# Kernel optimization log

Hardware: AMD Instinct MI355X
Metric: run time of the kernel (lower is better)

The kernel has to match this reference:

```python
import jax, jax.numpy as jnp
import numpy as np

N_NODES = 100000
N_EDGES = 1600000
DIMS = [128, 128, 128, 64]


def setup_inputs() -> dict:
    key = jax.random.key(0)
    ks = jax.random.split(key, 12)
    inp = {
        "features": jax.random.normal(ks[0], (N_NODES, DIMS[0]), dtype=jnp.float32),
        "src": jax.random.randint(ks[1], (N_EDGES,), 0, N_NODES, dtype=jnp.int64),
        "dst": jax.random.randint(ks[2], (N_EDGES,), 0, N_NODES, dtype=jnp.int64),
        "edge_weight": jax.random.uniform(ks[3], (N_EDGES,), dtype=jnp.float32),
    }
    # GraphConv weights (xavier-like scale) and biases per layer
    for i in range(3):
        fin, fout = DIMS[i], DIMS[i + 1]
        scale = (2.0 / (fin + fout)) ** 0.5
        inp[f"W{i}"] = jax.random.normal(ks[4 + i], (fin, fout), dtype=jnp.float32) * scale
        inp[f"b{i}"] = jnp.zeros((fout,), dtype=jnp.float32)
    return inp


def _graph_conv(h, W, b, src, dst, ew, out_norm, in_norm):
    # DGL GraphConv, norm='both', with per-edge weight (u_mul_e message).
    fin, fout = W.shape
    h = h * out_norm[:, None]
    if fin > fout:  # mult W first to reduce message width
        h = h @ W
    msg = h[src] * ew[:, None]                       # [E, d] irregular gather
    agg = jax.ops.segment_sum(msg, dst, num_segments=N_NODES)
    agg = agg * in_norm[:, None]
    if fin <= fout:
        agg = agg @ W
    return agg + b


def reference(features, src, dst, edge_weight, W0, b0, W1, b1, W2, b2):
    ones = jnp.ones((N_EDGES,), dtype=features.dtype)
    out_deg = jax.ops.segment_sum(ones, src, num_segments=N_NODES)
    in_deg = jax.ops.segment_sum(ones, dst, num_segments=N_NODES)
    out_norm = jnp.clip(out_deg, 1.0, None) ** -0.5
    in_norm = jnp.clip(in_deg, 1.0, None) ** -0.5
    h = features
    Ws = [(W0, b0), (W1, b1), (W2, b2)]
    for i, (W, b) in enumerate(Ws):
        h = _graph_conv(h, W, b, src, dst, edge_weight, out_norm, in_norm)
        if i < len(Ws) - 1:
            h = jax.nn.relu(h)
    return h
```

## Files before the change

### kernel.cpp

```cpp
#include <hip/hip_runtime.h>
#include <cstddef>
#include <cstdint>

typedef float f4 __attribute__((ext_vector_type(4)));
typedef unsigned long long u64;
typedef unsigned short u16;
typedef unsigned char u8;
typedef unsigned short u16x8 __attribute__((ext_vector_type(8)));
typedef short short8 __attribute__((ext_vector_type(8)));

__device__ __forceinline__ u64 ldnt8(const void* p) {
    return __builtin_nontemporal_load((const u64*)(p));
}
__device__ __forceinline__ u16 bfrn(float f) {
    unsigned u = __float_as_uint(f);
    return (u16)((u + 0x7FFFu + ((u >> 16) & 1u)) >> 16);
}
__device__ __forceinline__ float bl(unsigned w) { return __uint_as_float(w << 16); }
__device__ __forceinline__ float bh(unsigned w) { return __uint_as_float(w & 0xFFFF0000u); }


#define EPB 4096

__global__ void __launch_bounds__(256)
k_prep0(const int* __restrict__ src, const int* __restrict__ dst,
        int* __restrict__ bh_s, int* __restrict__ bh_d,
        const float* __restrict__ feat, u16* __restrict__ featb, int n8,
        const float* __restrict__ W0, const float* __restrict__ W1,
        const float* __restrict__ W2, u16* __restrict__ Wt0,
        u16* __restrict__ Wt1, u16* __restrict__ Wt2,
        int NB, int B1, int E) {
    const int bid = blockIdx.x, t = threadIdx.x;
    if (bid < B1) {
        __shared__ int hs[512], hd[512];
        for (int i = t; i < 512; i += 256) { hs[i] = 0; hd[i] = 0; }
        __syncthreads();
        const int e0 = bid * EPB;
        #pragma unroll
        for (int j = 0; j < 4; ++j) {
            const int e = e0 + j * 1024 + t * 4;
            if (e + 4 <= E) {
                const int4 d = *(const int4*)&dst[e];
                const int4 s = *(const int4*)&src[e];
                atomicAdd(&hd[d.x >> 8], 1);
                atomicAdd(&hd[d.y >> 8], 1);
                atomicAdd(&hd[d.z >> 8], 1);
                atomicAdd(&hd[d.w >> 8], 1);
                atomicAdd(&hs[s.x >> 8], 1);
                atomicAdd(&hs[s.y >> 8], 1);
                atomicAdd(&hs[s.z >> 8], 1);
                atomicAdd(&hs[s.w >> 8], 1);
            } else {
                for (int k = e; k < E && k < e + 4; ++k) {
                    atomicAdd(&hd[dst[k] >> 8], 1);
                    atomicAdd(&hs[src[k] >> 8], 1);
                }
            }
        }
        __syncthreads();
        for (int i = t; i < NB; i += 256) {
            bh_d[bid * NB + i] = hd[i];
            bh_s[bid * NB + i] = hs[i];
        }
    } else if (bid < B1 + (n8 + 255) / 256) {
        const int i = (bid - B1) * 256 + t;
        if (i < n8) {
            const f4 v0 = *(const f4*)(feat + (size_t)i * 8);
            const f4 v1 = *(const f4*)(feat + (size_t)i * 8 + 4);
            u16x8 r = {bfrn(v0.x), bfrn(v0.y), bfrn(v0.z), bfrn(v0.w),
                       bfrn(v1.x), bfrn(v1.y), bfrn(v1.z), bfrn(v1.w)};
            *(u16x8*)(featb + (size_t)i * 8) = r;
        }
    } else {
        const int i = (bid - B1 - (n8 + 255) / 256) * 256 + t;
        if (i < 16384) {
            const int k = i >> 7, c = i & 127;
            Wt0[c * 128 + k] = bfrn(W0[i]);
        } else if (i < 32768) {
            const int j = i - 16384, k = j >> 7, c = j & 127;
            Wt1[c * 128 + k] = bfrn(W1[j]);
        } else if (i < 40960) {
            const int j = i - 32768, k = j >> 6, c = j & 63;
            Wt2[c * 128 + k] = bfrn(W2[j]);
        }
    }
}

__global__ void __launch_bounds__(512)
k_p2(int* __restrict__ bh_d, int* __restrict__ bh_s,
     int* __restrict__ cb_d, int* __restrict__ cb_s, int NB, int B1) {
    __shared__ int tile[512][17];
    __shared__ int tot[16];
    const int t = threadIdx.x, lane = t & 63, wave = t >> 6;
    int* bh = blockIdx.y ? bh_s : bh_d;
    int* cb = blockIdx.y ? cb_s : cb_d;
    const int B0 = blockIdx.x * 16;
    #pragma unroll
    for (int j = 0; j < 16; ++j) {
        const int idx = j * 512 + t;
        const int row = idx >> 4, col = idx & 15;
        int v = 0;
        if (row < B1 && B0 + col < NB) v = bh[row * NB + B0 + col];
        tile[row][col] = v;
    }
    __syncthreads();
    #pragma unroll
    for (int cc = 0; cc < 2; ++cc) {
        const int col = wave * 2 + cc;
        int carry = 0;
        #pragma unroll
        for (int ch = 0; ch < 8; ++ch) {
            const int v = tile[ch * 64 + lane][col];
            int s = v;
            #pragma unroll
            for (int d = 1; d < 64; d <<= 1) {
                const int u = __shfl_up(s, d);
                if (lane >= d) s += u;
            }
            tile[ch * 64 + lane][col] = s - v + carry;
            carry += __shfl(s, 63);
        }
        if (lane == 0) tot[col] = carry;
    }
    __syncthreads();
    #pragma unroll
    for (int j = 0; j < 16; ++j) {
        const int idx = j * 512 + t;
        const int row = idx >> 4, col = idx & 15;
        if (row < B1 && B0 + col < NB) bh[row * NB + B0 + col] = tile[row][col];
    }
    if (t < 16 && B0 + t < NB) cb[B0 + t] = tot[t];
}

__global__ void __launch_bounds__(512)
k_p2b(const int* __restrict__ cb_d, const int* __restrict__ cb_s,
      int* __restrict__ bktb_d, int* __restrict__ bktb_s,
      int* __restrict__ row, int NB, int N, int E) {
    __shared__ int s[512];
    const int t = threadIdx.x;
    int v = (t < NB) ? cb_d[t] : 0;
    s[t] = v;
    __syncthreads();
    for (int off = 1; off < 512; off <<= 1) {
        const int x = (t >= off) ? s[t - off] : 0;
        __syncthreads();
        s[t] += x;
        __syncthreads();
    }
    if (t < NB) bktb_d[t] = s[t] - v;
    __syncthreads();
    v = (t < NB) ? cb_s[t] : 0;
    s[t] = v;
    __syncthreads();
    for (int off = 1; off < 512; off <<= 1) {
        const int x = (t >= off) ? s[t - off] : 0;
        __syncthreads();
        s[t] += x;
        __syncthreads();
    }
    if (t < NB) bktb_s[t] = s[t] - v;
    if (t == 0) row[N] = E;
}

__global__ void __launch_bounds__(256)
k_p3(const int* __restrict__ src, const int* __restrict__ dst,
     const float* __restrict__ ew,
     const int* __restrict__ bh_s, const int* __restrict__ bh_d,
     const int* __restrict__ bktb_s, const int* __restrict__ bktb_d,
     int2* __restrict__ tsw, u8* __restrict__ tsrc, int NB, int E) {
    __shared__ int hs[512], hd[512], base_s[512], base_d[512];
    const int t = threadIdx.x, b = blockIdx.x;
    for (int i = t; i < 512; i += 256) {
        hs[i] = 0; hd[i] = 0;
        if (i < NB) {
            base_d[i] = bktb_d[i] + bh_d[b * NB + i];
            base_s[i] = bktb_s[i] + bh_s[b * NB + i];
        }
    }
    __syncthreads();
    const int e0 = b * EPB;
    #pragma unroll
    for (int j = 0; j < 4; ++j) {
        const int e = e0 + j * 1024 + t * 4;
        if (e + 4 <= E) {
            const int4 d = *(const int4*)&dst[e];
            const int4 s = *(const int4*)&src[e];
            const f4   w = *(const f4*)&ew[e];
            const int dd[4] = {d.x, d.y, d.z, d.w};
            const int ss[4] = {s.x, s.y, s.z, s.w};
            const float ww[4] = {w.x, w.y, w.z, w.w};
            #pragma unroll
            for (int k = 0; k < 4; ++k) {
                const int Bd = dd[k] >> 8;
                const int rd = atomicAdd(&hd[Bd], 1);
                tsw[base_d[Bd] + rd] = make_int2(ss[k] | ((dd[k] & 255) << 24),
                                                 __float_as_int(ww[k]));
                const int Bs = ss[k] >> 8;
                const int rs = atomicAdd(&hs[Bs], 1);
                tsrc[base_s[Bs] + rs] = (u8)(ss[k] & 255);
            }
        } else {
            for (int k = e; k < E && k < e + 4; ++k) {
                const int dv = dst[k], sv = src[k];
                const int Bd = dv >> 8;
                const int rd = atomicAdd(&hd[Bd], 1);
                tsw[base_d[Bd] + rd] = make_int2(sv | ((dv & 255) << 24),
                                                 __float_as_int(ew[k]));
                const int Bs = sv >> 8;
                const int rs = atomicAdd(&hs[Bs], 1);
                tsrc[base_s[Bs] + rs] = (u8)(sv & 255);
            }
        }
    }
}

__global__ void __launch_bounds__(256)
k_p4s(const u8* __restrict__ tsrc, const int* __restrict__ bktb_s,
      const int* __restrict__ cb_s, float* __restrict__ onorm, int NB, int N) {
    __shared__ int cnt[256];
    const int B = blockIdx.x, t = threadIdx.x;
    cnt[t] = 0;
    __syncthreads();
    const int base = bktb_s[B], cb = cb_s[B];
    for (int i = t; i < cb; i += 256) atomicAdd(&cnt[tsrc[base + i]], 1);
    __syncthreads();
    const int n = (B << 8) + t;
    if (n < N) {
        const int c = cnt[t];
        onorm[n] = rsqrtf((float)(c < 1 ? 1 : c));
    }
}

__global__ void __launch_bounds__(256)
k_p4d(const int2* __restrict__ tsw,
      const int* __restrict__ bktb_d, const int* __restrict__ cb_d,
      const float* __restrict__ onorm, int* __restrict__ row,
      float* __restrict__ inorm, int2* __restrict__ csr, int NB, int N) {
    __shared__ int cnt[256], cnt2[256], lrow[256], sc[256];
    const int B = blockIdx.x, t = threadIdx.x;
    cnt[t] = 0; cnt2[t] = 0;
    __syncthreads();
    const int base = bktb_d[B], cb = cb_d[B];
    for (int i = t; i < cb; i += 256)
        atomicAdd(&cnt[((unsigned)tsw[base + i].x) >> 24], 1);
    __syncthreads();
    const int v = cnt[t];
    sc[t] = v;
    __syncthreads();
    for (int off = 1; off < 256; off <<= 1) {
        const int x = (t >= off) ? sc[t - off] : 0;
        __syncthreads();
        sc[t] += x;
        __syncthreads();
    }
    const int excl = sc[t] - v;
    lrow[t] = excl;
    const int n = (B << 8) + t;
    if (n < N) {
        row[n] = base + excl;
        inorm[n] = rsqrtf((float)(v < 1 ? 1 : v));
    }
    __syncthreads();
    for (int i = t; i < cb; i += 256) {
        const int2 sw = tsw[base + i];
        const int d = ((unsigned)sw.x) >> 24;
        const int s = sw.x & 0xFFFFFF;
        const int r = atomicAdd(&cnt2[d], 1);
        const float coef = __int_as_float(sw.y) * onorm[s];
        csr[base + lrow[d] + r] = make_int2(s, __float_as_int(coef));
    }
}

__global__ void __launch_bounds__(256)
k_agg128b(const u16* __restrict__ h, const int* __restrict__ row,
          const int2* __restrict__ csr, const float* __restrict__ inorm,
          u16* __restrict__ out, int N) {
    const int node = (int)((blockIdx.x * blockDim.x + threadIdx.x) >> 6);
    if (node >= N) return;
    const int lane = threadIdx.x & 63;
    const int q = lane >> 4;
    const int col = (lane & 15) * 8;
    int p = row[node];
    const int e = row[node + 1];
    float a0 = 0, a1 = 0, a2 = 0, a3 = 0, a4 = 0, a5 = 0, a6 = 0, a7 = 0;
    for (; p + 16 <= e; p += 16) {
        const u64 c0 = ldnt8(&csr[p + q]);
        const u64 c1 = ldnt8(&csr[p + 4 + q]);
        const u64 c2 = ldnt8(&csr[p + 8 + q]);
        const u64 c3 = ldnt8(&csr[p + 12 + q]);
        const uint4 w0 = *(const uint4*)(h + (size_t)(int)c0 * 128 + col);
        const uint4 w1 = *(const uint4*)(h + (size_t)(int)c1 * 128 + col);
        const uint4 w2 = *(const uint4*)(h + (size_t)(int)c2 * 128 + col);
        const uint4 w3 = *(const uint4*)(h + (size_t)(int)c3 * 128 + col);
        const float f0 = __int_as_float((int)(c0 >> 32));
        const float f1 = __int_as_float((int)(c1 >> 32));
        const float f2 = __int_as_float((int)(c2 >> 32));
        const float f3 = __int_as_float((int)(c3 >> 32));
        a0 = fmaf(f0, bl(w0.x), a0); a1 = fmaf(f0, bh(w0.x), a1);
        a2 = fmaf(f0, bl(w0.y), a2); a3 = fmaf(f0, bh(w0.y), a3);
        a4 = fmaf(f0, bl(w0.z), a4); a5 = fmaf(f0, bh(w0.z), a5);
        a6 = fmaf(f0, bl(w0.w), a6); a7 = fmaf(f0, bh(w0.w), a7);
        a0 = fmaf(f1, bl(w1.x), a0); a1 = fmaf(f1, bh(w1.x), a1);
        a2 = fmaf(f1, bl(w1.y), a2); a3 = fmaf(f1, bh(w1.y), a3);
        a4 = fmaf(f1, bl(w1.z), a4); a5 = fmaf(f1, bh(w1.z), a5);
        a6 = fmaf(f1, bl(w1.w), a6); a7 = fmaf(f1, bh(w1.w), a7);
        a0 = fmaf(f2, bl(w2.x), a0); a1 = fmaf(f2, bh(w2.x), a1);
        a2 = fmaf(f2, bl(w2.y), a2); a3 = fmaf(f2, bh(w2.y), a3);
        a4 = fmaf(f2, bl(w2.z), a4); a5 = fmaf(f2, bh(w2.z), a5);
        a6 = fmaf(f2, bl(w2.w), a6); a7 = fmaf(f2, bh(w2.w), a7);
        a0 = fmaf(f3, bl(w3.x), a0); a1 = fmaf(f3, bh(w3.x), a1);
        a2 = fmaf(f3, bl(w3.y), a2); a3 = fmaf(f3, bh(w3.y), a3);
        a4 = fmaf(f3, bl(w3.z), a4); a5 = fmaf(f3, bh(w3.z), a5);
        a6 = fmaf(f3, bl(w3.w), a6); a7 = fmaf(f3, bh(w3.w), a7);
    }
    for (; p + 8 <= e; p += 8) {
        const u64 c0 = ldnt8(&csr[p + q]);
        const u64 c1 = ldnt8(&csr[p + 4 + q]);
        const uint4 w0 = *(const uint4*)(h + (size_t)(int)c0 * 128 + col);
        const uint4 w1 = *(const uint4*)(h + (size_t)(int)c1 * 128 + col);
        const float f0 = __int_as_float((int)(c0 >> 32));
        const float f1 = __int_as_float((int)(c1 >> 32));
        a0 = fmaf(f0, bl(w0.x), a0); a1 = fmaf(f0, bh(w0.x), a1);
        a2 = fmaf(f0, bl(w0.y), a2); a3 = fmaf(f0, bh(w0.y), a3);
        a4 = fmaf(f0, bl(w0.z), a4); a5 = fmaf(f0, bh(w0.z), a5);
        a6 = fmaf(f0, bl(w0.w), a6); a7 = fmaf(f0, bh(w0.w), a7);
        a0 = fmaf(f1, bl(w1.x), a0); a1 = fmaf(f1, bh(w1.x), a1);
        a2 = fmaf(f1, bl(w1.y), a2); a3 = fmaf(f1, bh(w1.y), a3);
        a4 = fmaf(f1, bl(w1.z), a4); a5 = fmaf(f1, bh(w1.z), a5);
        a6 = fmaf(f1, bl(w1.w), a6); a7 = fmaf(f1, bh(w1.w), a7);
    }
    {
        const int i0 = p + q, i1 = p + 4 + q;
        if (i0 < e) {
            const u64 c = ldnt8(&csr[i0]);
            const uint4 w = *(const uint4*)(h + (size_t)(int)c * 128 + col);
            const float f = __int_as_float((int)(c >> 32));
            a0 = fmaf(f, bl(w.x), a0); a1 = fmaf(f, bh(w.x), a1);
            a2 = fmaf(f, bl(w.y), a2); a3 = fmaf(f, bh(w.y), a3);
            a4 = fmaf(f, bl(w.z), a4); a5 = fmaf(f, bh(w.z), a5);
            a6 = fmaf(f, bl(w.w), a6); a7 = fmaf(f, bh(w.w), a7);
        }
        if (i1 < e) {
            const u64 c = ldnt8(&csr[i1]);
            const uint4 w = *(const uint4*)(h + (size_t)(int)c * 128 + col);
            const float f = __int_as_float((int)(c >> 32));
            a0 = fmaf(f, bl(w.x), a0); a1 = fmaf(f, bh(w.x), a1);
            a2 = fmaf(f, bl(w.y), a2); a3 = fmaf(f, bh(w.y), a3);
            a4 = fmaf(f, bl(w.z), a4); a5 = fmaf(f, bh(w.z), a5);
            a6 = fmaf(f, bl(w.w), a6); a7 = fmaf(f, bh(w.w), a7);
        }
    }
    a0 += __shfl_xor(a0, 16); a1 += __shfl_xor(a1, 16);
    a2 += __shfl_xor(a2, 16); a3 += __shfl_xor(a3, 16);
    a4 += __shfl_xor(a4, 16); a5 += __shfl_xor(a5, 16);
    a6 += __shfl_xor(a6, 16); a7 += __shfl_xor(a7, 16);
    a0 += __shfl_xor(a0, 32); a1 += __shfl_xor(a1, 32);
    a2 += __shfl_xor(a2, 32); a3 += __shfl_xor(a3, 32);
    a4 += __shfl_xor(a4, 32); a5 += __shfl_xor(a5, 32);
    a6 += __shfl_xor(a6, 32); a7 += __shfl_xor(a7, 32);
    if (lane < 16) {
        const float nn = inorm[node];
        u16x8 r = {bfrn(a0 * nn), bfrn(a1 * nn), bfrn(a2 * nn), bfrn(a3 * nn),
                   bfrn(a4 * nn), bfrn(a5 * nn), bfrn(a6 * nn), bfrn(a7 * nn)};
        *(u16x8*)(out + (size_t)node * 128 + col) = r;
    }
}

__global__ void __launch_bounds__(256)
k_agg64b(const u16* __restrict__ h, const int* __restrict__ row,
         const int2* __restrict__ csr, const float* __restrict__ inorm,
         const float* __restrict__ bias, float* __restrict__ out, int N) {
    const int node = (int)((blockIdx.x * blockDim.x + threadIdx.x) >> 6);
    if (node >= N) return;
    const int lane = threadIdx.x & 63;
    const int oc = lane >> 3;
    const int col = (lane & 7) * 8;
    int p = row[node];
    const int e = row[node + 1];
    float a0 = 0, a1 = 0, a2 = 0, a3 = 0, a4 = 0, a5 = 0, a6 = 0, a7 = 0;
    for (; p + 16 <= e; p += 16) {
        const u64 c0 = ldnt8(&csr[p + oc]);
        const u64 c1 = ldnt8(&csr[p + 8 + oc]);
        const uint4 w0 = *(const uint4*)(h + (size_t)(int)c0 * 64 + col);
        const uint4 w1 = *(const uint4*)(h + (size_t)(int)c1 * 64 + col);
        const float f0 = __int_as_float((int)(c0 >> 32));
        const float f1 = __int_as_float((int)(c1 >> 32));
        a0 = fmaf(f0, bl(w0.x), a0); a1 = fmaf(f0, bh(w0.x), a1);
        a2 = fmaf(f0, bl(w0.y), a2); a3 = fmaf(f0, bh(w0.y), a3);
        a4 = fmaf(f0, bl(w0.z), a4); a5 = fmaf(f0, bh(w0.z), a5);
        a6 = fmaf(f0, bl(w0.w), a6); a7 = fmaf(f0, bh(w0.w), a7);
        a0 = fmaf(f1, bl(w1.x), a0); a1 = fmaf(f1, bh(w1.x), a1);
        a2 = fmaf(f1, bl(w1.y), a2); a3 = fmaf(f1, bh(w1.y), a3);
        a4 = fmaf(f1, bl(w1.z), a4); a5 = fmaf(f1, bh(w1.z), a5);
        a6 = fmaf(f1, bl(w1.w), a6); a7 = fmaf(f1, bh(w1.w), a7);
    }
    {
        const int i0 = p + oc, i1 = p + 8 + oc;
        if (i0 < e) {
            const u64 c = ldnt8(&csr[i0]);
            const uint4 w = *(const uint4*)(h + (size_t)(int)c * 64 + col);
            const float f = __int_as_float((int)(c >> 32));
            a0 = fmaf(f, bl(w.x), a0); a1 = fmaf(f, bh(w.x), a1);
            a2 = fmaf(f, bl(w.y), a2); a3 = fmaf(f, bh(w.y), a3);
            a4 = fmaf(f, bl(w.z), a4); a5 = fmaf(f, bh(w.z), a5);
            a6 = fmaf(f, bl(w.w), a6); a7 = fmaf(f, bh(w.w), a7);
        }
        if (i1 < e) {
            const u64 c = ldnt8(&csr[i1]);
            const uint4 w = *(const uint4*)(h + (size_t)(int)c * 64 + col);
            const float f = __int_as_float((int)(c >> 32));
            a0 = fmaf(f, bl(w.x), a0); a1 = fmaf(f, bh(w.x), a1);
            a2 = fmaf(f, bl(w.y), a2); a3 = fmaf(f, bh(w.y), a3);
            a4 = fmaf(f, bl(w.z), a4); a5 = fmaf(f, bh(w.z), a5);
            a6 = fmaf(f, bl(w.w), a6); a7 = fmaf(f, bh(w.w), a7);
        }
    }
    a0 += __shfl_xor(a0, 8);  a1 += __shfl_xor(a1, 8);
    a2 += __shfl_xor(a2, 8);  a3 += __shfl_xor(a3, 8);
    a4 += __shfl_xor(a4, 8);  a5 += __shfl_xor(a5, 8);
    a6 += __shfl_xor(a6, 8);  a7 += __shfl_xor(a7, 8);
    a0 += __shfl_xor(a0, 16); a1 += __shfl_xor(a1, 16);
    a2 += __shfl_xor(a2, 16); a3 += __shfl_xor(a3, 16);
    a4 += __shfl_xor(a4, 16); a5 += __shfl_xor(a5, 16);
    a6 += __shfl_xor(a6, 16); a7 += __shfl_xor(a7, 16);
    a0 += __shfl_xor(a0, 32); a1 += __shfl_xor(a1, 32);
    a2 += __shfl_xor(a2, 32); a3 += __shfl_xor(a3, 32);
    a4 += __shfl_xor(a4, 32); a5 += __shfl_xor(a5, 32);
    a6 += __shfl_xor(a6, 32); a7 += __shfl_xor(a7, 32);
    if (lane < 8) {
        const float nn = inorm[node];
        const f4 b0 = *(const f4*)(bias + col);
        const f4 b1 = *(const f4*)(bias + col + 4);
        f4 r0 = {a0 * nn + b0.x, a1 * nn + b0.y, a2 * nn + b0.z, a3 * nn + b0.w};
        f4 r1 = {a4 * nn + b1.x, a5 * nn + b1.y, a6 * nn + b1.z, a7 * nn + b1.w};
        *(f4*)(out + (size_t)node * 64 + col) = r0;
        *(f4*)(out + (size_t)node * 64 + col + 4) = r1;
    }
}

template <int COLS, bool RELU, bool BIAS>
__global__ void __launch_bounds__(256)
k_mgemm(const u16* __restrict__ A, const u16* __restrict__ Wt,
        const float* __restrict__ bias, u16* __restrict__ C, int N) {
    __shared__ u16 Wl[COLS][136];
    const int t = threadIdx.x;
    const int lane = t & 63;
    const int wave = t >> 6;
    #pragma unroll
    for (int i = 0; i < COLS / 16; ++i) {
        const int elem = (i * 256 + t) * 8;
        const int r = elem >> 7, c0 = elem & 127;
        *(short8*)&Wl[r][c0] = *(const short8*)(Wt + elem);
    }
    const int row0 = blockIdx.x * 64 + wave * 16;
    const int arow = min(row0 + (lane & 15), N - 1);
    const int koff = (lane >> 4) * 8;
    short8 a[4];
    #pragma unroll
    for (int kk = 0; kk < 4; ++kk)
        a[kk] = *(const short8*)(A + (size_t)arow * 128 + kk * 32 + koff);
    __syncthreads();

    f4 acc[COLS / 16];
    #pragma unroll
    for (int ct = 0; ct < COLS / 16; ++ct) acc[ct] = (f4){0.f, 0.f, 0.f, 0.f};

    #pragma unroll
    for (int ct = 0; ct < COLS / 16; ++ct) {
        #pragma unroll
        for (int kk = 0; kk < 4; ++kk) {
            const short8 b = *(const short8*)&Wl[ct * 16 + (lane & 15)][kk * 32 + koff];
            acc[ct] = __builtin_amdgcn_mfma_f32_16x16x32_bf16(a[kk], b, acc[ct], 0, 0, 0);
        }
    }

    #pragma unroll
    for (int ct = 0; ct < COLS / 16; ++ct) {
        const int c = ct * 16 + (lane & 15);
        const float bb = BIAS ? bias[c] : 0.f;
        #pragma unroll
        for (int r = 0; r < 4; ++r) {
            const int gr = row0 + (lane >> 4) * 4 + r;
            if (gr < N) {
                float v = acc[ct][r] + bb;
                if (RELU) v = v > 0.f ? v : 0.f;
                C[(size_t)gr * COLS + c] = bfrn(v);
            }
        }
    }
}

extern "C" void kernel_launch(void* const* d_in, const int* in_sizes, int n_in,
                              void* d_out, int out_size, void* d_ws, size_t ws_size,
                              hipStream_t stream) {
    const float* feat = (const float*)d_in[0];
    const int*   src  = (const int*)d_in[1];
    const int*   dst  = (const int*)d_in[2];
    const float* ew   = (const float*)d_in[3];
    const float* W0   = (const float*)d_in[4];
    const float* b0   = (const float*)d_in[5];
    const float* W1   = (const float*)d_in[6];
    const float* b1   = (const float*)d_in[7];
    const float* W2   = (const float*)d_in[8];
    const float* b2   = (const float*)d_in[9];
    float* out = (float*)d_out;

    const int N = in_sizes[0] / 128;
    const int E = in_sizes[1];
    const int NB = (N + 255) / 256;
    const int B1 = (E + EPB - 1) / EPB;
    const int n8 = N * 16;

    uint8_t* wp = (uint8_t*)d_ws;
    auto alloc = [&](size_t bytes) {
        uint8_t* r = wp;
        wp += (bytes + 511) & ~(size_t)511;
        return r;
    };
    u16*   featb = (u16*)alloc((size_t)N * 128 * 2);
    u16*   Xb    = (u16*)alloc((size_t)N * 128 * 2);
    u16*   Tb    = (u16*)alloc((size_t)N * 128 * 2);
    u8*    scr   = (u8*)alloc((size_t)E * 10 + 65536);
    int2*  csr   = (int2*)alloc((size_t)E * 8);
    int*   row   = (int*)alloc((size_t)(N + 1) * 4);
    float* onorm = (float*)alloc((size_t)N * 4);
    float* inorm = (float*)alloc((size_t)N * 4);
    u16*   Wt0   = (u16*)alloc(128 * 128 * 2);
    u16*   Wt1   = (u16*)alloc(128 * 128 * 2);
    u16*   Wt2   = (u16*)alloc(128 * 64 * 2);

    uint8_t* xp = (uint8_t*)Xb;
    auto xalloc = [&](size_t bytes) {
        uint8_t* r = xp;
        xp += (bytes + 511) & ~(size_t)511;
        return r;
    };
    int* bh_d   = (int*)xalloc((size_t)B1 * NB * 4);
    int* bh_s   = (int*)xalloc((size_t)B1 * NB * 4);
    int* cb_d   = (int*)xalloc((size_t)NB * 4);
    int* cb_s   = (int*)xalloc((size_t)NB * 4);
    int* bktb_d = (int*)xalloc((size_t)NB * 4);
    int* bktb_s = (int*)xalloc((size_t)NB * 4);

    uint8_t* yp = scr;
    auto yalloc = [&](size_t bytes) {
        uint8_t* r = yp;
        yp += (bytes + 511) & ~(size_t)511;
        return r;
    };
    int2* tsw  = (int2*)yalloc((size_t)E * 8);
    u8*   tsrc = (u8*)yalloc((size_t)E);
    u16*  Gb   = (u16*)scr;

    const int nbcvt = (n8 + 255) / 256;
    k_prep0<<<B1 + nbcvt + 160, 256, 0, stream>>>(
        src, dst, bh_s, bh_d, feat, featb, n8,
        W0, W1, W2, Wt0, Wt1, Wt2, NB, B1, E);
    k_p2<<<dim3((NB + 15) / 16, 2), 512, 0, stream>>>(bh_d, bh_s, cb_d, cb_s, NB, B1);
    k_p2b<<<1, 512, 0, stream>>>(cb_d, cb_s, bktb_d, bktb_s, row, NB, N, E);
    k_p3<<<B1, 256, 0, stream>>>(src, dst, ew, bh_s, bh_d, bktb_s, bktb_d,
                                 tsw, tsrc, NB, E);
    k_p4s<<<NB, 256, 0, stream>>>(tsrc, bktb_s, cb_s, onorm, NB, N);
    k_p4d<<<NB, 256, 0, stream>>>(tsw, bktb_d, cb_d, onorm, row, inorm, csr, NB, N);

    const int ab = (N + 3) / 4;
    const int gb = (N + 63) / 64;

    k_agg128b<<<ab, 256, 0, stream>>>(featb, row, csr, inorm, Tb, N);
    k_mgemm<128, true, true><<<gb, 256, 0, stream>>>(Tb, Wt0, b0, Xb, N);
    k_agg128b<<<ab, 256, 0, stream>>>(Xb, row, csr, inorm, Tb, N);
    k_mgemm<128, true, true><<<gb, 256, 0, stream>>>(Tb, Wt1, b1, featb, N);
    k_mgemm<64, false, false><<<gb, 256, 0, stream>>>(featb, Wt2, nullptr, Gb, N);
    k_agg64b<<<ab, 256, 0, stream>>>(Gb, row, csr, inorm, b2, out, N);
}
```

Baseline: 311.3 us.

## Fold source-degree norm into node features instead of per-edge CSR coefficients

Moves the out-degree normalisation off the per-edge CSR weights and applies it per node: the feature bf16 conversion is fused into the src-count kernel and pre-scaled by onorm, and the layer GEMM epilogues scale their outputs by onorm. The two p4 kernels merge into one launch with a 2D grid so the src and dst bucket work run concurrently. This removes the random gather of onorm per edge in CSR construction and one kernel launch. In exchange the feature conversion now waits for the degree pass instead of overlapping with the histogram, and rounding changes slightly because the norm is applied before bf16 conversion.

```diff
diff --git a/kernel.cpp b/kernel.cpp
--- a/kernel.cpp
+++ b/kernel.cpp
@@ -25,7 +25,6 @@
 __global__ void __launch_bounds__(256)
 k_prep0(const int* __restrict__ src, const int* __restrict__ dst,
         int* __restrict__ bh_s, int* __restrict__ bh_d,
-        const float* __restrict__ feat, u16* __restrict__ featb, int n8,
         const float* __restrict__ W0, const float* __restrict__ W1,
         const float* __restrict__ W2, u16* __restrict__ Wt0,
         u16* __restrict__ Wt1, u16* __restrict__ Wt2,
@@ -62,17 +61,8 @@
             bh_d[bid * NB + i] = hd[i];
             bh_s[bid * NB + i] = hs[i];
         }
-    } else if (bid < B1 + (n8 + 255) / 256) {
+    } else {
         const int i = (bid - B1) * 256 + t;
-        if (i < n8) {
-            const f4 v0 = *(const f4*)(feat + (size_t)i * 8);
-            const f4 v1 = *(const f4*)(feat + (size_t)i * 8 + 4);
-            u16x8 r = {bfrn(v0.x), bfrn(v0.y), bfrn(v0.z), bfrn(v0.w),
-                       bfrn(v1.x), bfrn(v1.y), bfrn(v1.z), bfrn(v1.w)};
-            *(u16x8*)(featb + (size_t)i * 8) = r;
-        }
-    } else {
-        const int i = (bid - B1 - (n8 + 255) / 256) * 256 + t;
         if (i < 16384) {
             const int k = i >> 7, c = i & 127;
             Wt0[c * 128 + k] = bfrn(W0[i]);
@@ -215,59 +205,73 @@
 }
 
 __global__ void __launch_bounds__(256)
-k_p4s(const u8* __restrict__ tsrc, const int* __restrict__ bktb_s,
-      const int* __restrict__ cb_s, float* __restrict__ onorm, int NB, int N) {
-    __shared__ int cnt[256];
+k_p4(const u8* __restrict__ tsrc, const int2* __restrict__ tsw,
+     const int* __restrict__ bktb_s, const int* __restrict__ cb_s,
+     const int* __restrict__ bktb_d, const int* __restrict__ cb_d,
+     const float* __restrict__ feat, u16* __restrict__ featb,
+     float* __restrict__ onorm, int* __restrict__ row,
+     float* __restrict__ inorm, int2* __restrict__ csr, int NB, int N) {
     const int B = blockIdx.x, t = threadIdx.x;
-    cnt[t] = 0;
-    __syncthreads();
-    const int base = bktb_s[B], cb = cb_s[B];
-    for (int i = t; i < cb; i += 256) atomicAdd(&cnt[tsrc[base + i]], 1);
-    __syncthreads();
-    const int n = (B << 8) + t;
-    if (n < N) {
+    if (blockIdx.y == 0) {
+        __shared__ int cnt[256];
+        __shared__ float nrm[256];
+        cnt[t] = 0;
+        __syncthreads();
+        const int base = bktb_s[B], cb = cb_s[B];
+        for (int i = t; i < cb; i += 256) atomicAdd(&cnt[tsrc[base + i]], 1);
+        __syncthreads();
+        const int n = (B << 8) + t;
         const int c = cnt[t];
-        onorm[n] = rsqrtf((float)(c < 1 ? 1 : c));
-    }
-}
-
-__global__ void __launch_bounds__(256)
-k_p4d(const int2* __restrict__ tsw,
-      const int* __restrict__ bktb_d, const int* __restrict__ cb_d,
-      const float* __restrict__ onorm, int* __restrict__ row,
-      float* __restrict__ inorm, int2* __restrict__ csr, int NB, int N) {
-    __shared__ int cnt[256], cnt2[256], lrow[256], sc[256];
-    const int B = blockIdx.x, t = threadIdx.x;
-    cnt[t] = 0; cnt2[t] = 0;
-    __syncthreads();
-    const int base = bktb_d[B], cb = cb_d[B];
-    for (int i = t; i < cb; i += 256)
-        atomicAdd(&cnt[((unsigned)tsw[base + i].x) >> 24], 1);
-    __syncthreads();
-    const int v = cnt[t];
-    sc[t] = v;
-    __syncthreads();
-    for (int off = 1; off < 256; off <<= 1) {
-        const int x = (t >= off) ? sc[t - off] : 0;
-        __syncthreads();
-        sc[t] += x;
-        __syncthreads();
-    }
-    const int excl = sc[t] - v;
-    lrow[t] = excl;
-    const int n = (B << 8) + t;
-    if (n < N) {
-        row[n] = base + excl;
-        inorm[n] = rsqrtf((float)(v < 1 ? 1 : v));
-    }
-    __syncthreads();
-    for (int i = t; i < cb; i += 256) {
-        const int2 sw = tsw[base + i];
-        const int d = ((unsigned)sw.x) >> 24;
-        const int s = sw.x & 0xFFFFFF;
-        const int r = atomicAdd(&cnt2[d], 1);
-        const float coef = __int_as_float(sw.y) * onorm[s];
-        csr[base + lrow[d] + r] = make_int2(s, __float_as_int(coef));
+        const float o = rsqrtf((float)(c < 1 ? 1 : c));
+        nrm[t] = o;
+        if (n < N) onorm[n] = o;
+        __syncthreads();
+        const int n0 = B << 8;
+        for (int idx = t; idx < 256 * 16; idx += 256) {
+            const int node = idx >> 4, g = idx & 15;
+            const int gn = n0 + node;
+            if (gn < N) {
+                const float o2 = nrm[node];
+                const f4 v0 = *(const f4*)(feat + (size_t)gn * 128 + g * 8);
+                const f4 v1 = *(const f4*)(feat + (size_t)gn * 128 + g * 8 + 4);
+                u16x8 r = {bfrn(v0.x * o2), bfrn(v0.y * o2),
+                           bfrn(v0.z * o2), bfrn(v0.w * o2),
+                           bfrn(v1.x * o2), bfrn(v1.y * o2),
+                           bfrn(v1.z * o2), bfrn(v1.w * o2)};
+                *(u16x8*)(featb + (size_t)gn * 128 + g * 8) = r;
+            }
+        }
+    } else {
+        __shared__ int cnt[256], cnt2[256], lrow[256], sc[256];
+        cnt[t] = 0; cnt2[t] = 0;
+        __syncthreads();
+        const int base = bktb_d[B], cb = cb_d[B];
+        for (int i = t; i < cb; i += 256)
+            atomicAdd(&cnt[((unsigned)tsw[base + i].x) >> 24], 1);
+        __syncthreads();
+        const int v = cnt[t];
+        sc[t] = v;
+        __syncthreads();
+        for (int off = 1; off < 256; off <<= 1) {
+            const int x = (t >= off) ? sc[t - off] : 0;
+            __syncthreads();
+            sc[t] += x;
+            __syncthreads();
+        }
+        const int excl = sc[t] - v;
+        lrow[t] = excl;
+        const int n = (B << 8) + t;
+        if (n < N) {
+            row[n] = base + excl;
+            inorm[n] = rsqrtf((float)(v < 1 ? 1 : v));
+        }
+        __syncthreads();
+        for (int i = t; i < cb; i += 256) {
+            const int2 sw = tsw[base + i];
+            const int d = ((unsigned)sw.x) >> 24;
+            const int r = atomicAdd(&cnt2[d], 1);
+            csr[base + lrow[d] + r] = make_int2(sw.x & 0xFFFFFF, sw.y);
+        }
     }
 }
 
@@ -438,10 +442,11 @@
     }
 }
 
-template <int COLS, bool RELU, bool BIAS>
+template <int COLS, bool RELU, bool BIAS, bool NORM>
 __global__ void __launch_bounds__(256)
 k_mgemm(const u16* __restrict__ A, const u16* __restrict__ Wt,
-        const float* __restrict__ bias, u16* __restrict__ C, int N) {
+        const float* __restrict__ bias, const float* __restrict__ norm,
+        u16* __restrict__ C, int N) {
     __shared__ u16 Wl[COLS][136];
     const int t = threadIdx.x;
     const int lane = t & 63;
@@ -472,6 +477,13 @@
             const short8 b = *(const short8*)&Wl[ct * 16 + (lane & 15)][kk * 32 + koff];
             acc[ct] = __builtin_amdgcn_mfma_f32_16x16x32_bf16(a[kk], b, acc[ct], 0, 0, 0);
         }
+    }
+
+    float nr[4];
+    #pragma unroll
+    for (int r = 0; r < 4; ++r) {
+        const int gr = row0 + (lane >> 4) * 4 + r;
+        nr[r] = (NORM && gr < N) ? norm[gr] : 1.f;
     }
 
     #pragma unroll
@@ -484,6 +496,7 @@
             if (gr < N) {
                 float v = acc[ct][r] + bb;
                 if (RELU) v = v > 0.f ? v : 0.f;
+                if (NORM) v *= nr[r];
                 C[(size_t)gr * COLS + c] = bfrn(v);
             }
         }
@@ -509,7 +522,6 @@
     const int E = in_sizes[1];
     const int NB = (N + 255) / 256;
     const int B1 = (E + EPB - 1) / EPB;
-    const int n8 = N * 16;
 
     uint8_t* wp = (uint8_t*)d_ws;
     auto alloc = [&](size_t bytes) {
@@ -552,24 +564,23 @@
     u8*   tsrc = (u8*)yalloc((size_t)E);
     u16*  Gb   = (u16*)scr;
 
-    const int nbcvt = (n8 + 255) / 256;
-    k_prep0<<<B1 + nbcvt + 160, 256, 0, stream>>>(
-        src, dst, bh_s, bh_d, feat, featb, n8,
-        W0, W1, W2, Wt0, Wt1, Wt2, NB, B1, E);
+    k_prep0<<<B1 + 160, 256, 0, stream>>>(src, dst, bh_s, bh_d,
+                                          W0, W1, W2, Wt0, Wt1, Wt2, NB, B1, E);
     k_p2<<<dim3((NB + 15) / 16, 2), 512, 0, stream>>>(bh_d, bh_s, cb_d, cb_s, NB, B1);
     k_p2b<<<1, 512, 0, stream>>>(cb_d, cb_s, bktb_d, bktb_s, row, NB, N, E);
     k_p3<<<B1, 256, 0, stream>>>(src, dst, ew, bh_s, bh_d, bktb_s, bktb_d,
                                  tsw, tsrc, NB, E);
-    k_p4s<<<NB, 256, 0, stream>>>(tsrc, bktb_s, cb_s, onorm, NB, N);
-    k_p4d<<<NB, 256, 0, stream>>>(tsw, bktb_d, cb_d, onorm, row, inorm, csr, NB, N);
+    k_p4<<<dim3(NB, 2), 256, 0, stream>>>(tsrc, tsw, bktb_s, cb_s, bktb_d, cb_d,
+                                          feat, featb, onorm, row, inorm, csr,
+                                          NB, N);
 
     const int ab = (N + 3) / 4;
     const int gb = (N + 63) / 64;
 
     k_agg128b<<<ab, 256, 0, stream>>>(featb, row, csr, inorm, Tb, N);
-    k_mgemm<128, true, true><<<gb, 256, 0, stream>>>(Tb, Wt0, b0, Xb, N);
+    k_mgemm<128, true, true, true><<<gb, 256, 0, stream>>>(Tb, Wt0, b0, onorm, Xb, N);
     k_agg128b<<<ab, 256, 0, stream>>>(Xb, row, csr, inorm, Tb, N);
-    k_mgemm<128, true, true><<<gb, 256, 0, stream>>>(Tb, Wt1, b1, featb, N);
-    k_mgemm<64, false, false><<<gb, 256, 0, stream>>>(featb, Wt2, nullptr, Gb, N);
+    k_mgemm<128, true, true, true><<<gb, 256, 0, stream>>>(Tb, Wt1, b1, onorm, featb, N);
+    k_mgemm<64, false, false, false><<<gb, 256, 0, stream>>>(featb, Wt2, nullptr, nullptr, Gb, N);
     k_agg64b<<<ab, 256, 0, stream>>>(Gb, row, csr, inorm, b2, out, N);
 }
```

After: 303.2 us. 1.03x faster.
